# Optimization experiments

Hardware: AMD Instinct MI355X
Metric: run time of the kernel (lower is better)

## Reference

```python
import jax, jax.numpy as jnp
import numpy as np
import math

N_HEAD = 16

def setup_inputs() -> dict:
    key = jax.random.key(0)
    ks = jax.random.split(key, 5)
    B, T, C = 4, 2048, 2048
    s = 1.0 / math.sqrt(C)
    return {
        "x": jax.random.normal(ks[0], (B, T, C), jnp.float32),
        "w_attn": jax.random.normal(ks[1], (C, 3 * C), jnp.float32) * s,
        "b_attn": jax.random.normal(ks[2], (3 * C,), jnp.float32) * 0.01,
        "w_proj": jax.random.normal(ks[3], (C, C), jnp.float32) * s,
        "b_proj": jax.random.normal(ks[4], (C,), jnp.float32) * 0.01,
    }

def reference(x, w_attn, b_attn, w_proj, b_proj):
    B, T, C = x.shape
    H = N_HEAD
    D = C // H
    # fused QKV projection: [B,T,3C] -> [3,B,H,T,D]
    qkv = (x @ w_attn + b_attn).reshape(B, T, 3, H, D).transpose(2, 0, 3, 1, 4)
    q, k, v = qkv[0], qkv[1], qkv[2]
    scale = 1.0 / math.sqrt(D)
    scores = jnp.einsum("bhqd,bhkd->bhqk", q, k) * scale  # [B,H,T,T]
    causal = jnp.tril(jnp.ones((T, T), dtype=bool))
    neg = jnp.finfo(scores.dtype).min
    scores = jnp.where(causal, scores, neg)
    attn = jax.nn.softmax(scores, axis=-1)
    y = jnp.einsum("bhqk,bhkd->bhqd", attn, v)  # [B,H,T,D]
    y = y.transpose(0, 2, 1, 3).reshape(B, T, C)
    return y @ w_proj + b_proj
```

## Files before the change

### kernel.cpp

```cpp
#include <hip/hip_runtime.h>
#include <hip/hip_bf16.h>
#include <stdint.h>

typedef unsigned short u16;
typedef __bf16 bf16x8 __attribute__((ext_vector_type(8)));
typedef unsigned short u16x8 __attribute__((ext_vector_type(8)));
typedef float f32x4 __attribute__((ext_vector_type(4)));
typedef float f32x16 __attribute__((ext_vector_type(16)));

__device__ __forceinline__ float bf2f(u16 u){ union{float f; unsigned i;} v; v.i = ((unsigned)u)<<16; return v.f; }
__device__ __forceinline__ u16 f2bf(float f){ union{float f; unsigned i;} v; v.f=f; unsigned r = v.i + 0x7FFFu + ((v.i>>16)&1u); return (u16)(r>>16); }

__device__ __forceinline__ void async16(const void* g, void* l){
  __builtin_amdgcn_global_load_lds((const __attribute__((address_space(1))) void*)g,
                                   (__attribute__((address_space(3))) void*)l, 16, 0, 0);
}

__global__ __launch_bounds__(256) void cvt_f2b(const float* __restrict__ src, u16* __restrict__ dst, int n)
{
  int i = (blockIdx.x * 256 + threadIdx.x) * 4;
  if (i < n) {
    float4 v = *(const float4*)&src[i];
    ushort4 o;
    o.x = f2bf(v.x); o.y = f2bf(v.y); o.z = f2bf(v.z); o.w = f2bf(v.w);
    *(ushort4*)&dst[i] = o;
  }
}

__global__ __launch_bounds__(256) void transpose2d_f2b(const float* __restrict__ src, u16* __restrict__ dst,
                                                       int src_rows, int src_cols)
{
  __shared__ u16 tile[64][72];
  const int r0 = blockIdx.y << 6, c0 = blockIdx.x << 6;
  const int t = threadIdx.x;
  #pragma unroll
  for (int i=0;i<4;i++){
    int slot = t + (i<<8);
    int r = slot >> 4, cv = (slot & 15) << 2;
    float4 v = *(const float4*)&src[(size_t)(r0+r)*src_cols + c0 + cv];
    tile[r][cv+0] = f2bf(v.x); tile[r][cv+1] = f2bf(v.y);
    tile[r][cv+2] = f2bf(v.z); tile[r][cv+3] = f2bf(v.w);
  }
  __syncthreads();
  #pragma unroll
  for (int i=0;i<2;i++){
    int slot = t + (i<<8);
    int cr = slot >> 3, rv = (slot & 7) << 3;
    u16x8 v;
    #pragma unroll
    for (int e=0;e<8;e++) v[e] = tile[rv+e][cr];
    *(u16x8*)&dst[(size_t)(c0+cr)*src_rows + r0 + rv] = v;
  }
}

__global__ __launch_bounds__(256) void transpose_v(const u16* __restrict__ qkv, u16* __restrict__ vt)
{
  __shared__ u16 tile[64][72];
  const int bh = blockIdx.z;
  const int b = bh >> 4, h = bh & 15;
  const u16* src = qkv + (size_t)b*2048*6144 + 4096 + h*128;
  u16* dst = vt + (size_t)bh*128*2048;
  const int t0 = blockIdx.y << 6, d0 = blockIdx.x << 6;
  const int t = threadIdx.x;
  #pragma unroll
  for (int i=0;i<2;i++){
    int slot = t + (i<<8);
    int r = slot >> 3, cv = (slot & 7) << 3;
    *(u16x8*)&tile[r][cv] = *(const u16x8*)&src[(size_t)(t0+r)*6144 + d0 + cv];
  }
  __syncthreads();
  #pragma unroll
  for (int i=0;i<2;i++){
    int slot = t + (i<<8);
    int cr = slot >> 3, rv = (slot & 7) << 3;
    u16x8 v;
    #pragma unroll
    for (int e=0;e<8;e++) v[e] = tile[rv+e][cr];
    *(u16x8*)&dst[(size_t)(d0+cr)*2048 + t0 + rv] = v;
  }
}

template<int F32OUT>
__global__ __launch_bounds__(512, 2) void gemm8p(const u16* __restrict__ A, const u16* __restrict__ Bt,
                                                 const float* __restrict__ bias, void* __restrict__ Cv,
                                                 int M, int N, int K, int ntn)
{
  __shared__ u16 lsA[2][2][256*32];
  __shared__ u16 lsB[2][2][256*32];
  const int tid = threadIdx.x;
  const int w = tid >> 6, lane = tid & 63;
  const int wm = w >> 2, wn = w & 3;
  const int l5 = lane >> 5, l31 = lane & 31;

  const int nwg = gridDim.x;
  const int bid = blockIdx.x;
  const int swz = (bid & 7) * (nwg >> 3) + (bid >> 3);
  const int nt = swz % ntn, mt = swz / ntn;
  const int m0 = mt << 8, n0 = nt << 8;
  const int NT = K >> 6, NI = NT >> 1;

  const int s0 = tid, s1 = tid + 512;
  const size_t off0 = (size_t)(s0>>2)*K + (size_t)((((s0&3) ^ ((s0>>3)&3))) << 3);
  const size_t off1 = (size_t)(s1>>2)*K + (size_t)((((s1&3) ^ ((s1>>3)&3))) << 3);
  const u16* Asrc = A + (size_t)m0*K;
  const u16* Bsrc = Bt + (size_t)n0*K;

  f32x16 acc[4][2];
  #pragma unroll
  for (int i=0;i<4;i++)
    #pragma unroll
    for (int j=0;j<2;j++)
      #pragma unroll
      for (int e=0;e<16;e++) acc[i][j][e] = 0.f;

  bf16x8 aE[4], aO[4], bX[4], bY[4];

#define SLOT(T, KH, AP, BP) do { \
    const u16* as_ = Asrc + (T)*64 + (KH)*32; \
    const u16* bs_ = Bsrc + (T)*64 + (KH)*32; \
    async16(as_ + off0, &(AP)[s0*8]); \
    async16(as_ + off1, &(AP)[s1*8]); \
    async16(bs_ + off0, &(BP)[s0*8]); \
    async16(bs_ + off1, &(BP)[s1*8]); \
  } while(0)

#define RDA(SET, BUF, KS, Q) do { \
    _Pragma("unroll") \
    for (int mb=0; mb<2; ++mb){ \
      int row_ = wm*128 + (Q)*64 + mb*32 + l31; \
      _Pragma("unroll") \
      for (int ks=0; ks<2; ++ks){ \
        int g_ = (ks*2 + l5) ^ ((row_>>1) & 3); \
        SET[mb*2+ks] = *(const bf16x8*)&lsA[BUF][KS][row_*32 + (g_<<3)]; \
      } \
    } } while(0)

#define RDB(SET, BUF, KS) do { \
    _Pragma("unroll") \
    for (int nb=0; nb<2; ++nb){ \
      int row_ = wn*64 + nb*32 + l31; \
      _Pragma("unroll") \
      for (int ks=0; ks<2; ++ks){ \
        int g_ = (ks*2 + l5) ^ ((row_>>1) & 3); \
        SET[nb*2+ks] = *(const bf16x8*)&lsB[BUF][KS][row_*32 + (g_<<3)]; \
      } \
    } } while(0)

#define MM(Q, AS, BS) do { \
    __builtin_amdgcn_s_setprio(1); \
    _Pragma("unroll") \
    for (int mb=0; mb<2; ++mb) \
      _Pragma("unroll") \
      for (int nb=0; nb<2; ++nb) \
        _Pragma("unroll") \
        for (int ks=0; ks<2; ++ks) \
          acc[(Q)*2+mb][nb] = __builtin_amdgcn_mfma_f32_32x32x16_bf16(AS[mb*2+ks], BS[nb*2+ks], acc[(Q)*2+mb][nb], 0,0,0); \
    __builtin_amdgcn_s_setprio(0); \
  } while(0)

#define LGK4 do { asm volatile("s_waitcnt lgkmcnt(4)" ::: "memory"); __builtin_amdgcn_sched_barrier(0); } while(0)
#define LGK8 do { asm volatile("s_waitcnt lgkmcnt(8)" ::: "memory"); __builtin_amdgcn_sched_barrier(0); } while(0)
#define LGK0 do { asm volatile("s_waitcnt lgkmcnt(0)" ::: "memory"); __builtin_amdgcn_sched_barrier(0); } while(0)
#define VM8 asm volatile("s_waitcnt vmcnt(8)" ::: "memory")
#define VM4 asm volatile("s_waitcnt vmcnt(4)" ::: "memory")
#define VM0 asm volatile("s_waitcnt vmcnt(0)" ::: "memory")
#define ENDP do { __builtin_amdgcn_s_barrier(); __builtin_amdgcn_sched_barrier(0); } while(0)

  SLOT(0, 0, lsA[0][0], lsB[0][0]);
  SLOT(0, 1, lsA[0][1], lsB[0][1]);
  SLOT(1, 0, lsA[1][0], lsB[1][0]);
  VM8;
  __builtin_amdgcn_s_barrier();
  __builtin_amdgcn_sched_barrier(0);
  RDA(aO, 0,0, 0); RDB(bX, 0,0);

  #pragma unroll 1
  for (int i = 0; i < NI-1; ++i){
    const int t0 = 2*i;
    RDA(aE, 0,0, 1); SLOT(t0+1,1, lsA[1][1], lsB[1][1]); LGK4; MM(0, aO, bX); VM8; ENDP;
    RDA(aO, 0,1, 0); RDB(bY, 0,1);                       LGK8; MM(1, aE, bX);      ENDP;
    RDA(aE, 0,1, 1); SLOT(t0+2,0, lsA[0][0], lsB[0][0]); LGK4; MM(0, aO, bY); VM8; ENDP;
    RDA(aO, 1,0, 0); RDB(bX, 1,0);                       LGK8; MM(1, aE, bY);      ENDP;
    RDA(aE, 1,0, 1); SLOT(t0+2,1, lsA[0][1], lsB[0][1]); LGK4; MM(0, aO, bX); VM8; ENDP;
    RDA(aO, 1,1, 0); RDB(bY, 1,1);                       LGK8; MM(1, aE, bX);      ENDP;
    RDA(aE, 1,1, 1); SLOT(t0+3,0, lsA[1][0], lsB[1][0]); LGK4; MM(0, aO, bY); VM8; ENDP;
    RDA(aO, 0,0, 0); RDB(bX, 0,0);                       LGK8; MM(1, aE, bY);      ENDP;
  }
  RDA(aE, 0,0, 1); SLOT(NT-1,1, lsA[1][1], lsB[1][1]);   LGK4; MM(0, aO, bX); VM8; ENDP;
  RDA(aO, 0,1, 0); RDB(bY, 0,1);                         LGK8; MM(1, aE, bX);      ENDP;
  RDA(aE, 0,1, 1);                                       LGK4; MM(0, aO, bY); VM4; ENDP;
  RDA(aO, 1,0, 0); RDB(bX, 1,0);                         LGK8; MM(1, aE, bY);      ENDP;
  RDA(aE, 1,0, 1);                                       LGK4; MM(0, aO, bX); VM0; ENDP;
  RDA(aO, 1,1, 0); RDB(bY, 1,1);                         LGK8; MM(1, aE, bX);      ENDP;
  RDA(aE, 1,1, 1);                                       LGK4; MM(0, aO, bY);      ENDP;
                                                         LGK0; MM(1, aE, bY);

#undef SLOT
#undef RDA
#undef RDB
#undef MM

  float bv[2];
  #pragma unroll
  for (int nb=0;nb<2;nb++) bv[nb] = bias[n0 + wn*64 + nb*32 + l31];
  #pragma unroll
  for (int am=0;am<4;am++){
    #pragma unroll
    for (int nb=0;nb<2;nb++){
      int col = n0 + wn*64 + nb*32 + l31;
      #pragma unroll
      for (int r=0;r<16;r++){
        int row = m0 + wm*128 + am*32 + (r&3) + 8*(r>>2) + 4*l5;
        float vv = acc[am][nb][r] + bv[nb];
        if (F32OUT) ((float*)Cv)[(size_t)row*N + col] = vv;
        else        ((u16*)Cv)[(size_t)row*N + col] = f2bf(vv);
      }
    }
  }
}

__global__ __launch_bounds__(512, 4) void attn_fwd(const u16* __restrict__ qkv, const u16* __restrict__ vt,
                                                   u16* __restrict__ y)
{
  __shared__ u16 kb[2][64*128];
  __shared__ u16 vb[2][128*64];
  __shared__ u16 plds[8][16*64];
  const int bh = blockIdx.x;
  const int b = bh >> 4, h = bh & 15;
  const int pair = blockIdx.y;
  const int tid = threadIdx.x;
  const int w = tid >> 6, lane = tid & 63;
  const int lo = lane & 15, hi = lane >> 4;

  const u16* Qb = qkv + (size_t)b*2048*6144 + h*128;
  const u16* Kb = Qb + 2048;
  const u16* Vb = vt + (size_t)bh*128*2048;
  u16* pw = &plds[w][0];
  const float sc = 0.08838834764831845f * 1.4426950408889634f;
  f32x4 z = {0.f,0.f,0.f,0.f};

  #pragma unroll 1
  for (int seg = 0; seg < 2; ++seg){
    const int qt = seg ? pair : 15 - pair;
    const int qw = qt*128 + w*16;
    const int nt = qt*2 + 2;

    bf16x8 qf[4];
    #pragma unroll
    for (int kd=0;kd<4;kd++)
      qf[kd] = *(const bf16x8*)&Qb[(size_t)(qw + lo)*6144 + kd*32 + hi*8];

    f32x4 o[8];
    #pragma unroll
    for (int dj=0;dj<8;dj++) o[dj] = z;
    float mx[4], lsum[4];
    #pragma unroll
    for (int r=0;r<4;r++){ mx[r] = -3.0e38f; lsum[r] = 0.f; }

    #pragma unroll
    for (int i=0;i<2;i++){
      int slot = i*512 + tid;
      int kr = slot >> 4;
      int kc = ((slot & 15) << 4) ^ ((kr & 7) << 4);
      async16(Kb + (size_t)kr*6144 + (kc >> 1), &kb[0][(size_t)(i*512 + w*64)*8]);
      int vr = slot >> 3;
      int vc = ((slot & 7) << 4) ^ ((vr & 7) << 4);
      async16(Vb + (size_t)vr*2048 + (vc >> 1), &vb[0][(size_t)(i*512 + w*64)*8]);
    }
    __syncthreads();

    #pragma unroll 1
    for (int it = 0; it < nt; ++it){
      const int k0 = it*64;
      if (it + 1 < nt){
        const int kn = (it+1)*64;
        u16* kdst = kb[(it+1)&1];
        u16* vdst = vb[(it+1)&1];
        #pragma unroll
        for (int i=0;i<2;i++){
          int slot = i*512 + tid;
          int kr = slot >> 4;
          int kc = ((slot & 15) << 4) ^ ((kr & 7) << 4);
          async16(Kb + (size_t)(kn + kr)*6144 + (kc >> 1), &kdst[(size_t)(i*512 + w*64)*8]);
          int vr = slot >> 3;
          int vc = ((slot & 7) << 4) ^ ((vr & 7) << 4);
          async16(Vb + (size_t)vr*2048 + kn + (vc >> 1), &vdst[(size_t)(i*512 + w*64)*8]);
        }
      }
      if (k0 <= qw + 15){
        const u16* kcur = kb[it&1];
        const u16* vcur = vb[it&1];
        f32x4 s[4];
        #pragma unroll
        for (int t=0;t<4;t++) s[t] = z;
        __builtin_amdgcn_s_setprio(1);
        #pragma unroll
        for (int t=0;t<4;t++){
          #pragma unroll
          for (int kd=0;kd<4;kd++){
            int row = t*16 + lo;
            int cb = (kd*64 + hi*16) ^ ((lo & 7) << 4);
            bf16x8 kk = *(const bf16x8*)&kcur[row*128 + (cb >> 1)];
            s[t] = __builtin_amdgcn_mfma_f32_16x16x32_bf16(qf[kd], kk, s[t], 0,0,0);
          }
        }
        __builtin_amdgcn_s_setprio(0);

        if (k0 + 63 > qw) {
          #pragma unroll
          for (int t=0;t<4;t++)
            #pragma unroll
            for (int r=0;r<4;r++){
              int q = qw + hi*4 + r;
              int k = k0 + t*16 + lo;
              if (k > q) s[t][r] = -3.0e38f;
            }
        }
        #pragma unroll
        for (int r=0;r<4;r++){
          float tm = fmaxf(fmaxf(s[0][r], s[1][r]), fmaxf(s[2][r], s[3][r]));
          tm = fmaxf(tm, __shfl_xor(tm, 1));
          tm = fmaxf(tm, __shfl_xor(tm, 2));
          tm = fmaxf(tm, __shfl_xor(tm, 4));
          tm = fmaxf(tm, __shfl_xor(tm, 8));
          tm *= sc;
          float mn = fmaxf(mx[r], tm);
          float al = exp2f(mx[r] - mn);
          mx[r] = mn;
          float p0 = exp2f(fmaf(s[0][r], sc, -mn));
          float p1 = exp2f(fmaf(s[1][r], sc, -mn));
          float p2 = exp2f(fmaf(s[2][r], sc, -mn));
          float p3 = exp2f(fmaf(s[3][r], sc, -mn));
          float sum = (p0 + p1) + (p2 + p3);
          sum += __shfl_xor(sum, 1);
          sum += __shfl_xor(sum, 2);
          sum += __shfl_xor(sum, 4);
          sum += __shfl_xor(sum, 8);
          lsum[r] = lsum[r]*al + sum;
          #pragma unroll
          for (int dj=0;dj<8;dj++) o[dj][r] *= al;
          int row = hi*4 + r;
          int sw = (row & 7) << 4;
          u16* prow = pw + row*64;
          prow[((     lo*2) ^ sw) >> 1] = f2bf(p0);
          prow[((32 + lo*2) ^ sw) >> 1] = f2bf(p1);
          prow[((64 + lo*2) ^ sw) >> 1] = f2bf(p2);
          prow[((96 + lo*2) ^ sw) >> 1] = f2bf(p3);
        }

        bf16x8 pa[2];
        #pragma unroll
        for (int kf=0;kf<2;kf++)
          pa[kf] = *(const bf16x8*)&pw[(lo*128 + ((kf*64 + hi*16) ^ ((lo & 7) << 4))) >> 1];
        __builtin_amdgcn_s_setprio(1);
        #pragma unroll
        for (int dj=0;dj<8;dj++){
          int row = dj*16 + lo;
          int cb0 = (hi*16)      ^ ((lo & 7) << 4);
          int cb1 = (64 + hi*16) ^ ((lo & 7) << 4);
          bf16x8 vv0 = *(const bf16x8*)&vcur[row*64 + (cb0 >> 1)];
          bf16x8 vv1 = *(const bf16x8*)&vcur[row*64 + (cb1 >> 1)];
          o[dj] = __builtin_amdgcn_mfma_f32_16x16x32_bf16(pa[0], vv0, o[dj], 0,0,0);
          o[dj] = __builtin_amdgcn_mfma_f32_16x16x32_bf16(pa[1], vv1, o[dj], 0,0,0);
        }
        __builtin_amdgcn_s_setprio(0);
      }
      __syncthreads();
    }

    #pragma unroll
    for (int r=0;r<4;r++){
      float inv = 1.0f / lsum[r];
      size_t row = (size_t)(b*2048 + qw + hi*4 + r);
      #pragma unroll
      for (int dj=0;dj<8;dj++)
        y[row*2048 + h*128 + dj*16 + lo] = f2bf(o[dj][r] * inv);
    }
    __syncthreads();
  }
}

extern "C" void kernel_launch(void* const* d_in, const int* in_sizes, int n_in,
                              void* d_out, int out_size, void* d_ws, size_t ws_size,
                              hipStream_t stream) {
  (void)in_sizes; (void)n_in; (void)out_size; (void)ws_size;
  const float* x      = (const float*)d_in[0];
  const float* w_attn = (const float*)d_in[1];
  const float* b_attn = (const float*)d_in[2];
  const float* w_proj = (const float*)d_in[3];
  const float* b_proj = (const float*)d_in[4];
  float* out = (float*)d_out;

  char* ws = (char*)d_ws;
  u16* xbf = (u16*)(ws);
  u16* wT  = (u16*)(ws + 33554432);
  u16* pT  = (u16*)(ws + 58720256);
  u16* qkv = (u16*)(ws + 67108864);
  u16* vt  = (u16*)(ws + 167772160);
  u16* y   = xbf;

  cvt_f2b<<<16384, 256, 0, stream>>>(x, xbf, 8192*2048);
  transpose2d_f2b<<<dim3(96,32), 256, 0, stream>>>(w_attn, wT, 2048, 6144);
  transpose2d_f2b<<<dim3(32,32), 256, 0, stream>>>(w_proj, pT, 2048, 2048);
  gemm8p<0><<<768, 512, 0, stream>>>(xbf, wT, b_attn, qkv, 8192, 6144, 2048, 24);
  transpose_v<<<dim3(2,32,64), 256, 0, stream>>>(qkv, vt);
  attn_fwd<<<dim3(64,8), 512, 0, stream>>>(qkv, vt, y);
  gemm8p<1><<<256, 512, 0, stream>>>(y, pT, b_proj, out, 8192, 2048, 2048, 8);
}
```

Measured before the change: 506.2 us.

## Switch attention kernel to 32x32x16 MFMA with 4 waves of 32 query rows

The attention kernel now uses 4 waves per block, each owning 32 query rows, and computes QK^T and PV with 32x32x16 bf16 MFMA instead of 16x16x32. K and V tiles are shared by fewer waves, so each wave reuses every LDS fragment over more rows, and the P staging buffer is resized to match. The aim is fewer LDS reads per FLOP and better MFMA efficiency. In exchange each thread holds more accumulator and softmax state, which adds register pressure and may lower occupancy, and the causal-skip granularity gets coarser.

```diff
diff --git a/kernel.cpp b/kernel.cpp
--- a/kernel.cpp
+++ b/kernel.cpp
@@ -219,53 +219,54 @@
   }
 }
 
-__global__ __launch_bounds__(512, 4) void attn_fwd(const u16* __restrict__ qkv, const u16* __restrict__ vt,
+__global__ __launch_bounds__(256, 2) void attn_fwd(const u16* __restrict__ qkv, const u16* __restrict__ vt,
                                                    u16* __restrict__ y)
 {
   __shared__ u16 kb[2][64*128];
   __shared__ u16 vb[2][128*64];
-  __shared__ u16 plds[8][16*64];
+  __shared__ u16 plds[4][32*64];
   const int bh = blockIdx.x;
   const int b = bh >> 4, h = bh & 15;
   const int pair = blockIdx.y;
   const int tid = threadIdx.x;
   const int w = tid >> 6, lane = tid & 63;
-  const int lo = lane & 15, hi = lane >> 4;
+  const int l31 = lane & 31, l5 = lane >> 5;
 
   const u16* Qb = qkv + (size_t)b*2048*6144 + h*128;
   const u16* Kb = Qb + 2048;
   const u16* Vb = vt + (size_t)bh*128*2048;
   u16* pw = &plds[w][0];
   const float sc = 0.08838834764831845f * 1.4426950408889634f;
-  f32x4 z = {0.f,0.f,0.f,0.f};
 
   #pragma unroll 1
   for (int seg = 0; seg < 2; ++seg){
     const int qt = seg ? pair : 15 - pair;
-    const int qw = qt*128 + w*16;
+    const int qw = qt*128 + w*32;
     const int nt = qt*2 + 2;
 
-    bf16x8 qf[4];
-    #pragma unroll
-    for (int kd=0;kd<4;kd++)
-      qf[kd] = *(const bf16x8*)&Qb[(size_t)(qw + lo)*6144 + kd*32 + hi*8];
-
-    f32x4 o[8];
-    #pragma unroll
-    for (int dj=0;dj<8;dj++) o[dj] = z;
-    float mx[4], lsum[4];
-    #pragma unroll
-    for (int r=0;r<4;r++){ mx[r] = -3.0e38f; lsum[r] = 0.f; }
-
-    #pragma unroll
-    for (int i=0;i<2;i++){
-      int slot = i*512 + tid;
-      int kr = slot >> 4;
-      int kc = ((slot & 15) << 4) ^ ((kr & 7) << 4);
-      async16(Kb + (size_t)kr*6144 + (kc >> 1), &kb[0][(size_t)(i*512 + w*64)*8]);
-      int vr = slot >> 3;
-      int vc = ((slot & 7) << 4) ^ ((vr & 7) << 4);
-      async16(Vb + (size_t)vr*2048 + (vc >> 1), &vb[0][(size_t)(i*512 + w*64)*8]);
+    bf16x8 qf[8];
+    #pragma unroll
+    for (int ds=0; ds<8; ds++)
+      qf[ds] = *(const bf16x8*)&Qb[(size_t)(qw + l31)*6144 + ds*16 + l5*8];
+
+    f32x16 o[4];
+    #pragma unroll
+    for (int nb=0;nb<4;nb++)
+      #pragma unroll
+      for (int e=0;e<16;e++) o[nb][e] = 0.f;
+    float mx[16], ls[16];
+    #pragma unroll
+    for (int r=0;r<16;r++){ mx[r] = -3.0e38f; ls[r] = 0.f; }
+
+    #pragma unroll
+    for (int j=0;j<4;j++){
+      int i = tid + j*256;
+      int kr = i >> 4;
+      int kc = ((i & 15) << 4) ^ ((kr & 7) << 4);
+      async16(Kb + (size_t)kr*6144 + (kc >> 1), &kb[0][(size_t)i*8]);
+      int vr = i >> 3;
+      int vc = ((i & 7) << 4) ^ ((vr & 7) << 4);
+      async16(Vb + (size_t)vr*2048 + (vc >> 1), &vb[0][(size_t)i*8]);
     }
     __syncthreads();
 
@@ -277,91 +278,91 @@
         u16* kdst = kb[(it+1)&1];
         u16* vdst = vb[(it+1)&1];
         #pragma unroll
-        for (int i=0;i<2;i++){
-          int slot = i*512 + tid;
-          int kr = slot >> 4;
-          int kc = ((slot & 15) << 4) ^ ((kr & 7) << 4);
-          async16(Kb + (size_t)(kn + kr)*6144 + (kc >> 1), &kdst[(size_t)(i*512 + w*64)*8]);
-          int vr = slot >> 3;
-          int vc = ((slot & 7) << 4) ^ ((vr & 7) << 4);
-          async16(Vb + (size_t)vr*2048 + kn + (vc >> 1), &vdst[(size_t)(i*512 + w*64)*8]);
+        for (int j=0;j<4;j++){
+          int i = tid + j*256;
+          int kr = i >> 4;
+          int kc = ((i & 15) << 4) ^ ((kr & 7) << 4);
+          async16(Kb + (size_t)(kn + kr)*6144 + (kc >> 1), &kdst[(size_t)i*8]);
+          int vr = i >> 3;
+          int vc = ((i & 7) << 4) ^ ((vr & 7) << 4);
+          async16(Vb + (size_t)vr*2048 + kn + (vc >> 1), &vdst[(size_t)i*8]);
         }
       }
-      if (k0 <= qw + 15){
+      if (k0 <= qw + 31){
         const u16* kcur = kb[it&1];
         const u16* vcur = vb[it&1];
-        f32x4 s[4];
-        #pragma unroll
-        for (int t=0;t<4;t++) s[t] = z;
+        f32x16 sA[2];
+        #pragma unroll
+        for (int nb=0;nb<2;nb++)
+          #pragma unroll
+          for (int e=0;e<16;e++) sA[nb][e] = 0.f;
         __builtin_amdgcn_s_setprio(1);
         #pragma unroll
-        for (int t=0;t<4;t++){
+        for (int ds=0; ds<8; ++ds){
           #pragma unroll
-          for (int kd=0;kd<4;kd++){
-            int row = t*16 + lo;
-            int cb = (kd*64 + hi*16) ^ ((lo & 7) << 4);
-            bf16x8 kk = *(const bf16x8*)&kcur[row*128 + (cb >> 1)];
-            s[t] = __builtin_amdgcn_mfma_f32_16x16x32_bf16(qf[kd], kk, s[t], 0,0,0);
+          for (int nb=0; nb<2; ++nb){
+            int krow = nb*32 + l31;
+            int cb = (ds*32 + l5*16) ^ ((krow & 7) << 4);
+            bf16x8 kk = *(const bf16x8*)&kcur[krow*128 + (cb >> 1)];
+            sA[nb] = __builtin_amdgcn_mfma_f32_32x32x16_bf16(qf[ds], kk, sA[nb], 0,0,0);
           }
         }
         __builtin_amdgcn_s_setprio(0);
 
         if (k0 + 63 > qw) {
           #pragma unroll
-          for (int t=0;t<4;t++)
+          for (int nb=0;nb<2;nb++)
             #pragma unroll
-            for (int r=0;r<4;r++){
-              int q = qw + hi*4 + r;
-              int k = k0 + t*16 + lo;
-              if (k > q) s[t][r] = -3.0e38f;
+            for (int r=0;r<16;r++){
+              int qrow = qw + (r&3) + 8*(r>>2) + 4*l5;
+              int kcol = k0 + nb*32 + l31;
+              if (kcol > qrow) sA[nb][r] = -3.0e38f;
             }
         }
         #pragma unroll
-        for (int r=0;r<4;r++){
-          float tm = fmaxf(fmaxf(s[0][r], s[1][r]), fmaxf(s[2][r], s[3][r]));
-          tm = fmaxf(tm, __shfl_xor(tm, 1));
-          tm = fmaxf(tm, __shfl_xor(tm, 2));
-          tm = fmaxf(tm, __shfl_xor(tm, 4));
-          tm = fmaxf(tm, __shfl_xor(tm, 8));
-          tm *= sc;
-          float mn = fmaxf(mx[r], tm);
+        for (int r=0;r<16;r++){
+          float tmv = fmaxf(sA[0][r], sA[1][r]);
+          tmv = fmaxf(tmv, __shfl_xor(tmv, 1));
+          tmv = fmaxf(tmv, __shfl_xor(tmv, 2));
+          tmv = fmaxf(tmv, __shfl_xor(tmv, 4));
+          tmv = fmaxf(tmv, __shfl_xor(tmv, 8));
+          tmv = fmaxf(tmv, __shfl_xor(tmv, 16));
+          tmv *= sc;
+          float mn = fmaxf(mx[r], tmv);
           float al = exp2f(mx[r] - mn);
           mx[r] = mn;
-          float p0 = exp2f(fmaf(s[0][r], sc, -mn));
-          float p1 = exp2f(fmaf(s[1][r], sc, -mn));
-          float p2 = exp2f(fmaf(s[2][r], sc, -mn));
-          float p3 = exp2f(fmaf(s[3][r], sc, -mn));
-          float sum = (p0 + p1) + (p2 + p3);
+          float p0 = exp2f(fmaf(sA[0][r], sc, -mn));
+          float p1 = exp2f(fmaf(sA[1][r], sc, -mn));
+          float sum = p0 + p1;
           sum += __shfl_xor(sum, 1);
           sum += __shfl_xor(sum, 2);
           sum += __shfl_xor(sum, 4);
           sum += __shfl_xor(sum, 8);
-          lsum[r] = lsum[r]*al + sum;
+          sum += __shfl_xor(sum, 16);
+          ls[r] = ls[r]*al + sum;
           #pragma unroll
-          for (int dj=0;dj<8;dj++) o[dj][r] *= al;
-          int row = hi*4 + r;
+          for (int nb=0;nb<4;nb++) o[nb][r] *= al;
+          int row = (r&3) + 8*(r>>2) + 4*l5;
           int sw = (row & 7) << 4;
-          u16* prow = pw + row*64;
-          prow[((     lo*2) ^ sw) >> 1] = f2bf(p0);
-          prow[((32 + lo*2) ^ sw) >> 1] = f2bf(p1);
-          prow[((64 + lo*2) ^ sw) >> 1] = f2bf(p2);
-          prow[((96 + lo*2) ^ sw) >> 1] = f2bf(p3);
-        }
-
-        bf16x8 pa[2];
-        #pragma unroll
-        for (int kf=0;kf<2;kf++)
-          pa[kf] = *(const bf16x8*)&pw[(lo*128 + ((kf*64 + hi*16) ^ ((lo & 7) << 4))) >> 1];
+          pw[(row*128 + (((l31*2)      ) ^ sw)) >> 1] = f2bf(p0);
+          pw[(row*128 + (((l31*2) + 64 ) ^ sw)) >> 1] = f2bf(p1);
+        }
+        bf16x8 pfr[4];
+        #pragma unroll
+        for (int ks=0; ks<4; ++ks){
+          int cb = (ks*32 + l5*16) ^ ((l31 & 7) << 4);
+          pfr[ks] = *(const bf16x8*)&pw[(l31*128 + cb) >> 1];
+        }
         __builtin_amdgcn_s_setprio(1);
         #pragma unroll
-        for (int dj=0;dj<8;dj++){
-          int row = dj*16 + lo;
-          int cb0 = (hi*16)      ^ ((lo & 7) << 4);
-          int cb1 = (64 + hi*16) ^ ((lo & 7) << 4);
-          bf16x8 vv0 = *(const bf16x8*)&vcur[row*64 + (cb0 >> 1)];
-          bf16x8 vv1 = *(const bf16x8*)&vcur[row*64 + (cb1 >> 1)];
-          o[dj] = __builtin_amdgcn_mfma_f32_16x16x32_bf16(pa[0], vv0, o[dj], 0,0,0);
-          o[dj] = __builtin_amdgcn_mfma_f32_16x16x32_bf16(pa[1], vv1, o[dj], 0,0,0);
+        for (int nb=0; nb<4; ++nb){
+          #pragma unroll
+          for (int ks=0; ks<4; ++ks){
+            int vrow = nb*32 + l31;
+            int cb = (ks*32 + l5*16) ^ ((vrow & 7) << 4);
+            bf16x8 vv = *(const bf16x8*)&vcur[vrow*64 + (cb >> 1)];
+            o[nb] = __builtin_amdgcn_mfma_f32_32x32x16_bf16(pfr[ks], vv, o[nb], 0,0,0);
+          }
         }
         __builtin_amdgcn_s_setprio(0);
       }
@@ -369,12 +370,12 @@
     }
 
     #pragma unroll
-    for (int r=0;r<4;r++){
-      float inv = 1.0f / lsum[r];
-      size_t row = (size_t)(b*2048 + qw + hi*4 + r);
+    for (int r=0;r<16;r++){
+      float inv = 1.0f / ls[r];
+      size_t row = (size_t)(b*2048 + qw + (r&3) + 8*(r>>2) + 4*l5);
       #pragma unroll
-      for (int dj=0;dj<8;dj++)
-        y[row*2048 + h*128 + dj*16 + lo] = f2bf(o[dj][r] * inv);
+      for (int nb=0;nb<4;nb++)
+        y[row*2048 + h*128 + nb*32 + l31] = f2bf(o[nb][r] * inv);
     }
     __syncthreads();
   }
@@ -404,6 +405,6 @@
   transpose2d_f2b<<<dim3(32,32), 256, 0, stream>>>(w_proj, pT, 2048, 2048);
   gemm8p<0><<<768, 512, 0, stream>>>(xbf, wT, b_attn, qkv, 8192, 6144, 2048, 24);
   transpose_v<<<dim3(2,32,64), 256, 0, stream>>>(qkv, vt);
-  attn_fwd<<<dim3(64,8), 512, 0, stream>>>(qkv, vt, y);
+  attn_fwd<<<dim3(64,8), 256, 0, stream>>>(qkv, vt, y);
   gemm8p<1><<<256, 512, 0, stream>>>(y, pT, b_proj, out, 8192, 2048, 2048, 8);
 }
```

After: 625.5 us. 23.6% more time.
